# Kernel tuning notes

Hardware: AMD Instinct MI355X
Metric: run time of the kernel (lower is better)

The kernel has to match this reference:

```python
import jax, jax.numpy as jnp
import numpy as np

RADIUS = 2
TEMP = 1.0
B, CIN, D, H, W = 1, 32, 64, 64, 64
PROJ, OUT = 64, 64
K = (2 * RADIUS + 1) ** 3  # 125 local offsets

_OFFSETS = np.array([(dz, dy, dx)
                     for dz in range(-RADIUS, RADIUS + 1)
                     for dy in range(-RADIUS, RADIUS + 1)
                     for dx in range(-RADIUS, RADIUS + 1)], dtype=np.int32)


def _conv3d(x, w, b, pad):
    y = jax.lax.conv_general_dilated(
        x, w, window_strides=(1, 1, 1), padding=[(pad, pad)] * 3,
        dimension_numbers=('NCDHW', 'OIDHW', 'NCDHW'))
    if b is not None:
        y = y + b[None, :, None, None, None]
    return y


def _l2norm(x):
    # torch F.normalize(dim=1): x / max(||x||_2, 1e-12)
    n = jnp.sqrt(jnp.sum(x * x, axis=1, keepdims=True))
    return x / jnp.maximum(n, 1e-12)


def _inorm(x, eps=1e-5):
    # InstanceNorm3d (affine=False): normalize over spatial dims per (B,C)
    mu = jnp.mean(x, axis=(2, 3, 4), keepdims=True)
    var = jnp.mean((x - mu) ** 2, axis=(2, 3, 4), keepdims=True)
    return (x - mu) * jax.lax.rsqrt(var + eps)


def _ntn(x):
    return jnp.nan_to_num(x, nan=0.0, posinf=0.0, neginf=0.0)


def setup_inputs() -> dict:
    key = jax.random.key(0)
    ks = jax.random.split(key, 8)
    s = 0.05
    return {
        'source_features': jax.random.normal(ks[0], (B, CIN, D, H, W), jnp.float32),
        'warped_target_features': jax.random.normal(ks[1], (B, CIN, D, H, W), jnp.float32),
        'w_src': jax.random.normal(ks[2], (PROJ, CIN, 1, 1, 1), jnp.float32) * s,
        'b_src': jnp.zeros((PROJ,), jnp.float32),
        'w_tgt': jax.random.normal(ks[3], (PROJ, CIN, 1, 1, 1), jnp.float32) * s,
        'b_tgt': jnp.zeros((PROJ,), jnp.float32),
        'w_enc1': jax.random.normal(ks[4], (OUT, K + 5, 3, 3, 3), jnp.float32) * s,
        'b_enc1': jnp.zeros((OUT,), jnp.float32),
        'w_enc2': jax.random.normal(ks[5], (OUT, OUT, 3, 3, 3), jnp.float32) * s,
        'b_enc2': jnp.zeros((OUT,), jnp.float32),
    }


def reference(source_features, warped_target_features, w_src, b_src, w_tgt, b_tgt,
              w_enc1, b_enc1, w_enc2, b_enc2):
    sp = _l2norm(_conv3d(source_features, w_src, b_src, 0))      # [B,P,D,H,W]
    tp = _l2norm(_conv3d(warped_target_features, w_tgt, b_tgt, 0))
    pt = jnp.pad(tp, ((0, 0), (0, 0), (RADIUS, RADIUS), (RADIUS, RADIUS), (RADIUS, RADIUS)),
                 mode='edge')  # replicate pad

    starts = jnp.asarray(_OFFSETS + RADIUS, jnp.int32)  # [K,3] slice starts

    def corr_one(st):
        sh = jax.lax.dynamic_slice(pt, (0, 0, st[0], st[1], st[2]), (B, PROJ, D, H, W))
        return jnp.sum(sp * sh, axis=1)  # [B,D,H,W]

    corr = jnp.transpose(jax.vmap(corr_one)(starts), (1, 0, 2, 3, 4))  # [B,K,D,H,W]
    scaled = corr / max(TEMP, 1e-6)

    top2 = jax.lax.top_k(jnp.moveaxis(scaled, 1, -1), 2)[0]  # [B,D,H,W,2]
    m = jnp.moveaxis(top2[..., 0:1], -1, 1)   # running max   [B,1,D,H,W]
    s2 = jnp.moveaxis(top2[..., 1:2], -1, 1)  # second max

    p = jnp.exp(scaled - m)                    # [B,K,D,H,W]
    Z = jnp.sum(p, axis=1, keepdims=True)
    inv = 1.0 / jnp.maximum(Z, 1e-8)

    offv = jnp.asarray(_OFFSETS, jnp.float32)  # [K,3]
    expected_offset = _ntn(jnp.einsum('bkdhw,kc->bcdhw', p, offv) * inv)
    confidence = _ntn(jnp.minimum(inv, 1.0))   # max-prob = exp(m-m)/Z
    second_prob = jnp.exp(s2 - m) * inv
    margin = _ntn(jnp.maximum(confidence - second_prob, 0.0))
    entropy = _ntn(m + jnp.log(jnp.maximum(Z, 1e-8))
                   - jnp.sum(p * scaled, axis=1, keepdims=True) * inv)

    enc_in = jnp.concatenate([corr, expected_offset, confidence, entropy], axis=1)  # [B,K+5,D,H,W]
    h = _conv3d(enc_in, w_enc1, b_enc1, 1)
    h = jax.nn.gelu(_inorm(h), approximate=False)
    h = _conv3d(h, w_enc2, b_enc2, 1)
    h = jax.nn.gelu(_inorm(h), approximate=False)
    encoded_features = _ntn(h)

    return expected_offset, confidence, margin, entropy, encoded_features
```

## Files before the change

kernel.cpp:

```cpp
#include <hip/hip_runtime.h>

#define DEV __device__ __forceinline__

typedef short bf16x8 __attribute__((ext_vector_type(8)));
typedef float f32x4 __attribute__((ext_vector_type(4)));
typedef float f32x16 __attribute__((ext_vector_type(16)));

static const int NVOX = 262144;

DEV float bflo(unsigned int u) { return __uint_as_float(u << 16); }
DEV float bfhi(unsigned int u) { return __uint_as_float(u & 0xffff0000u); }
DEV float bf2f(unsigned short s) { return __uint_as_float(((unsigned int)s) << 16); }
DEV unsigned short f2bf(float f) {
    unsigned int x = __float_as_uint(f);
    x += 0x7fffu + ((x >> 16) & 1u);
    return (unsigned short)(x >> 16);
}
DEV float ldin(const void* p, int i, int f) {
    return f ? ((const float*)p)[i] : bf2f(((const unsigned short*)p)[i]);
}

DEV void gld16(const unsigned short* g, unsigned short* l) {
    __builtin_amdgcn_global_load_lds(
        (const __attribute__((address_space(1))) unsigned int*)g,
        (__attribute__((address_space(3))) unsigned int*)l, 16, 0, 0);
}

__global__ void sniff_kernel(const unsigned short* __restrict__ src, int* __restrict__ flag) {
    __shared__ int cnt[256];
    int t = threadIdx.x;
    int c = 0;
    for (int i = t; i < 4096; i += 256) {
        unsigned int u = (unsigned int)src[i] & 0x7fffu;
        c += (u >= 0x4900u) ? 1 : 0;
    }
    cnt[t] = c;
    __syncthreads();
    for (int s = 128; s > 0; s >>= 1) {
        if (t < s) cnt[t] += cnt[t + s];
        __syncthreads();
    }
    if (t == 0) *flag = (cnt[0] > 8) ? 1 : 0;
}

__global__ void prep_kernel(const void* __restrict__ w1, const void* __restrict__ w2,
                            const void* __restrict__ bsv, const void* __restrict__ btv,
                            const void* __restrict__ b1v, const void* __restrict__ b2v,
                            const int* __restrict__ flag,
                            unsigned short* __restrict__ Wf1,
                            unsigned short* __restrict__ Wf2,
                            float* __restrict__ fbias) {
    const int f = *flag;
    int idx = blockIdx.x * 256 + threadIdx.x;
    const int N1  = 27 * 8 * 2 * 512;
    const int N1E = 4 * 2 * 512;
    const int N2  = 27 * 4 * 2 * 512;
    if (idx < N1) {
        int frag = idx >> 9;
        int r    = idx & 511;
        int lane = r >> 3, j = r & 7;
        int nt = frag & 1;
        int tk = frag >> 1;
        int tap = tk >> 3, kc = tk & 7;
        int o  = nt * 32 + (lane & 31);
        int cp = kc * 16 + (lane >> 5) * 8 + j;
        Wf1[idx] = f2bf(ldin(w1, (o * 130 + cp) * 27 + tap, f));
    } else if (idx < N1 + N1E) {
        int i2 = idx - N1;
        int frag = i2 >> 9;
        int r    = i2 & 511;
        int lane = r >> 3, j = r & 7;
        int nt = frag & 1, kc = frag >> 1;
        int o   = nt * 32 + (lane & 31);
        int kap = kc * 16 + (lane >> 5) * 8 + j;
        unsigned short val = 0;
        if (kap < 54) {
            int tap = kap >> 1, ch = 128 + (kap & 1);
            val = f2bf(ldin(w1, (o * 130 + ch) * 27 + tap, f));
        }
        Wf1[idx] = val;
    } else if (idx < N1 + N1E + N2) {
        int i2 = idx - N1 - N1E;
        int frag = i2 >> 9;
        int r    = i2 & 511;
        int lane = r >> 3, j = r & 7;
        int nt = frag & 1;
        int tk = frag >> 1;
        int tap = tk >> 2, kc = tk & 3;
        int o = nt * 32 + (lane & 31);
        int c = kc * 16 + (lane >> 5) * 8 + j;
        Wf2[i2] = f2bf(ldin(w2, (o * 64 + c) * 27 + tap, f));
    } else if (idx < N1 + N1E + N2 + 256) {
        int j = idx - N1 - N1E - N2;
        const void* bp = (j < 64) ? bsv : (j < 128) ? btv : (j < 192) ? b1v : b2v;
        fbias[j] = ldin(bp, j & 63, f);
    }
}

__global__ __launch_bounds__(256) void proj_kernel(
        const void* __restrict__ Xsrc, const void* __restrict__ Xtgt,
        const void* __restrict__ Wsrc, const void* __restrict__ Wtgt,
        const float* __restrict__ fbias, const int* __restrict__ flag,
        unsigned short* __restrict__ SP, unsigned short* __restrict__ TP) {
    const int f = *flag;
    const void* Xin = blockIdx.y ? Xtgt : Xsrc;
    const void* W   = blockIdx.y ? Wtgt : Wsrc;
    const float* Bb = fbias + (blockIdx.y ? 64 : 0);
    unsigned short* Outp = blockIdx.y ? TP : SP;

    __shared__ float ws[2048];
    const int t = threadIdx.x;
    for (int i = t; i < 2048; i += 256) {
        int ci = i >> 6, o = i & 63;
        ws[i] = ldin(W, o * 32 + ci, f);
    }
    __syncthreads();

    const size_t v = (size_t)blockIdx.x * 256 + t;
    float acc[64];
#pragma unroll
    for (int o = 0; o < 64; ++o) acc[o] = Bb[o];
    if (f) {
        const float* Xf = (const float*)Xin;
        for (int ci = 0; ci < 32; ++ci) {
            float x = Xf[(size_t)ci * NVOX + v];
            const float4* wr = (const float4*)(ws + ci * 64);
#pragma unroll
            for (int o4 = 0; o4 < 16; ++o4) {
                float4 w4 = wr[o4];
                acc[o4 * 4 + 0] = fmaf(w4.x, x, acc[o4 * 4 + 0]);
                acc[o4 * 4 + 1] = fmaf(w4.y, x, acc[o4 * 4 + 1]);
                acc[o4 * 4 + 2] = fmaf(w4.z, x, acc[o4 * 4 + 2]);
                acc[o4 * 4 + 3] = fmaf(w4.w, x, acc[o4 * 4 + 3]);
            }
        }
    } else {
        const unsigned short* Xb = (const unsigned short*)Xin;
        for (int ci = 0; ci < 32; ++ci) {
            float x = bf2f(Xb[(size_t)ci * NVOX + v]);
            const float4* wr = (const float4*)(ws + ci * 64);
#pragma unroll
            for (int o4 = 0; o4 < 16; ++o4) {
                float4 w4 = wr[o4];
                acc[o4 * 4 + 0] = fmaf(w4.x, x, acc[o4 * 4 + 0]);
                acc[o4 * 4 + 1] = fmaf(w4.y, x, acc[o4 * 4 + 1]);
                acc[o4 * 4 + 2] = fmaf(w4.z, x, acc[o4 * 4 + 2]);
                acc[o4 * 4 + 3] = fmaf(w4.w, x, acc[o4 * 4 + 3]);
            }
        }
    }
    float s = 0.f;
#pragma unroll
    for (int o = 0; o < 64; ++o) s = fmaf(acc[o], acc[o], s);
    float scale = 1.f / fmaxf(sqrtf(s), 1e-12f);

    unsigned int pk[32];
#pragma unroll
    for (int o = 0; o < 32; ++o)
        pk[o] = (unsigned int)f2bf(acc[2 * o] * scale) |
                ((unsigned int)f2bf(acc[2 * o + 1] * scale) << 16);
    uint4* outp = (uint4*)(Outp + v * 64);
#pragma unroll
    for (int j = 0; j < 8; ++j)
        outp[j] = make_uint4(pk[4 * j], pk[4 * j + 1], pk[4 * j + 2], pk[4 * j + 3]);
}

__global__ __launch_bounds__(256) void corr_kernel(
        const unsigned short* __restrict__ SP, const unsigned short* __restrict__ TP,
        unsigned short* __restrict__ X1, float* __restrict__ Out) {
    __shared__ __align__(16) unsigned short tpb[2][80 * 64];
    __shared__ __align__(16) unsigned short sband[2][64 * 128];

    const int t = threadIdx.x;
    const int wv = t >> 6, lane = t & 63;
    const int q = lane >> 4, l16 = lane & 15;
    const int x0 = wv * 16;

    const int bid = blockIdx.x;
    const int wg = (bid & 7) * 256 + (bid >> 3);
    const int z = wg >> 5, y = (wg & 31) * 2;
    const size_t vb0 = ((size_t)z * 64 + y) * 64;
    const size_t vb1 = vb0 + 64;

    const unsigned short* ar0 = SP + (vb0 + x0 + l16) * 64 + q * 8;
    const unsigned short* ar1 = SP + (vb1 + x0 + l16) * 64 + q * 8;
    const bf16x8 a00 = *(const bf16x8*)(ar0);
    const bf16x8 a01 = *(const bf16x8*)(ar0 + 32);
    const bf16x8 a10 = *(const bf16x8*)(ar1);
    const bf16x8 a11 = *(const bf16x8*)(ar1 + 32);

    auto stage_tp = [&](int it, int b) {
        const int zc = min(max(z + it / 6 - 2, 0), 63);
        const int yc = min(max(y - 2 + it % 6, 0), 63);
        const unsigned short* tb = TP + ((size_t)zc * 64 + yc) * 4096;
#pragma unroll
        for (int j = 0; j < 2; ++j) {
            int c = t + j * 256;
            int pp = c >> 3, cc = c & 7;
            int xc = min(max(pp - 2, 0), 63);
            gld16(tb + xc * 64 + ((cc ^ (pp & 7)) * 8),
                  &tpb[b][(wv * 64 + j * 256) * 8]);
        }
        if (wv < 2) {
            int c = 512 + wv * 64 + lane;
            int pp = c >> 3, cc = c & 7;
            int xc = min(max(pp - 2, 0), 63);
            gld16(tb + xc * 64 + ((cc ^ (pp & 7)) * 8),
                  &tpb[b][(512 + wv * 64) * 8]);
        }
    };

    stage_tp(0, 0);
    __syncthreads();

    int p = 0;
    for (int it = 0; it < 30; ++it) {
        if (it < 29) stage_tp(it + 1, p ^ 1);
        const int dz = it / 6, j = it % 6;
        const bool r0 = (j < 5), r1 = (j > 0);

        f32x4 acc0[2] = {{0.f, 0.f, 0.f, 0.f}, {0.f, 0.f, 0.f, 0.f}};
        f32x4 acc1[2] = {{0.f, 0.f, 0.f, 0.f}, {0.f, 0.f, 0.f, 0.f}};
        {
            const char* tb = (const char*)tpb[p];
#pragma unroll
            for (int nt = 0; nt < 2; ++nt) {
                const int pr = x0 + nt * 16 + l16;
                bf16x8 b0 = *(const bf16x8*)(tb + pr * 128 + ((q ^ (pr & 7)) * 16));
                bf16x8 b1 = *(const bf16x8*)(tb + pr * 128 + (((4 + q) ^ (pr & 7)) * 16));
                if (r0) {
                    acc0[nt] = __builtin_amdgcn_mfma_f32_16x16x32_bf16(a00, b0, acc0[nt], 0, 0, 0);
                    acc0[nt] = __builtin_amdgcn_mfma_f32_16x16x32_bf16(a01, b1, acc0[nt], 0, 0, 0);
                }
                if (r1) {
                    acc1[nt] = __builtin_amdgcn_mfma_f32_16x16x32_bf16(a10, b0, acc1[nt], 0, 0, 0);
                    acc1[nt] = __builtin_amdgcn_mfma_f32_16x16x32_bf16(a11, b1, acc1[nt], 0, 0, 0);
                }
            }
        }
        if (r0) {
            const int kb = dz * 25 + j * 5;
            char* sg = (char*)sband[0];
#pragma unroll
            for (int nt = 0; nt < 2; ++nt)
#pragma unroll
                for (int r = 0; r < 4; ++r) {
                    int ml = q * 4 + r;
                    int dxp = nt * 16 + l16 - ml;
                    if ((unsigned)dxp < 5u) {
                        int xl = x0 + ml;
                        *(unsigned short*)(sg + xl * 256 + (((kb + dxp) * 2) ^ ((xl & 7) << 4))) =
                            f2bf(acc0[nt][r]);
                    }
                }
        }
        if (r1) {
            const int kb = dz * 25 + (j - 1) * 5;
            char* sg = (char*)sband[1];
#pragma unroll
            for (int nt = 0; nt < 2; ++nt)
#pragma unroll
                for (int r = 0; r < 4; ++r) {
                    int ml = q * 4 + r;
                    int dxp = nt * 16 + l16 - ml;
                    if ((unsigned)dxp < 5u) {
                        int xl = x0 + ml;
                        *(unsigned short*)(sg + xl * 256 + (((kb + dxp) * 2) ^ ((xl & 7) << 4))) =
                            f2bf(acc1[nt][r]);
                    }
                }
        }
        __syncthreads();
        p ^= 1;
    }

    for (int half = 0; half < 2; ++half) {
        const size_t vbase = half ? vb1 : vb0;
        const int vox = t >> 2, part = t & 3;
        const int sx = (vox & 7) << 4;
        const char* sg = (const char*)sband[half];
        uint4 u[4];
#pragma unroll
        for (int j = 0; j < 4; ++j)
            u[j] = *(const uint4*)(sg + vox * 256 + ((part * 64 + j * 16) ^ sx));

        float m = -1e30f, s2 = -1e30f;
#pragma unroll
        for (int j = 0; j < 4; ++j) {
            const unsigned int uu[4] = {u[j].x, u[j].y, u[j].z, u[j].w};
#pragma unroll
            for (int w = 0; w < 4; ++w) {
                int k = part * 32 + j * 8 + w * 2;
                float d0 = (k < 125) ? bflo(uu[w]) : -1e30f;
                float d1 = (k + 1 < 125) ? bfhi(uu[w]) : -1e30f;
                float lo0 = fminf(d0, m); m = fmaxf(d0, m); s2 = fmaxf(s2, lo0);
                float lo1 = fminf(d1, m); m = fmaxf(d1, m); s2 = fmaxf(s2, lo1);
            }
        }
#pragma unroll
        for (int off = 1; off <= 2; off <<= 1) {
            float om = __shfl_xor(m, off, 64);
            float os = __shfl_xor(s2, off, 64);
            float lo = fminf(m, om);
            m = fmaxf(m, om);
            s2 = fmaxf(fmaxf(s2, os), lo);
        }
        int kk = part * 32;
        int dz0 = kk / 25, rem = kk - dz0 * 25, dy0 = rem / 5, dx0 = rem - dy0 * 5;
        float fx = (float)(dx0 - 2), fy = (float)(dy0 - 2), fz = (float)(dz0 - 2);
        float Zs = 0.f, S1 = 0.f, Ox = 0.f, Oy = 0.f, Oz = 0.f;
#pragma unroll
        for (int j = 0; j < 4; ++j) {
            const unsigned int uu[4] = {u[j].x, u[j].y, u[j].z, u[j].w};
#pragma unroll
            for (int w = 0; w < 8; ++w) {
                int k = part * 32 + j * 8 + w;
                bool ok = (k < 125);
                float d = (w & 1) ? bfhi(uu[w >> 1]) : bflo(uu[w >> 1]);
                d = ok ? d : 0.f;
                float e = ok ? __expf(d - m) : 0.f;
                Zs += e; S1 = fmaf(e, d, S1);
                Ox = fmaf(e, fx, Ox); Oy = fmaf(e, fy, Oy); Oz = fmaf(e, fz, Oz);
                fx += 1.f;
                if (fx > 2.5f) { fx = -2.f; fy += 1.f; if (fy > 2.5f) { fy = -2.f; fz += 1.f; } }
            }
        }
#pragma unroll
        for (int off = 1; off <= 2; off <<= 1) {
            Zs += __shfl_xor(Zs, off, 64);
            S1 += __shfl_xor(S1, off, 64);
            Ox += __shfl_xor(Ox, off, 64);
            Oy += __shfl_xor(Oy, off, 64);
            Oz += __shfl_xor(Oz, off, 64);
        }
        if (part == 0) {
            float inv  = 1.f / fmaxf(Zs, 1e-8f);
            float eoz = Oz * inv, eoy = Oy * inv, eox = Ox * inv;
            float conf = fminf(inv, 1.f);
            float marg = fmaxf(conf - __expf(s2 - m) * inv, 0.f);
            float ent  = m + __logf(fmaxf(Zs, 1e-8f)) - S1 * inv;
            char* sgw = (char*)sband[half];
            *(unsigned short*)(sgw + vox * 256 + (250 ^ sx)) = f2bf(eoz);
            *(unsigned short*)(sgw + vox * 256 + (252 ^ sx)) = f2bf(eoy);
            *(unsigned short*)(sgw + vox * 256 + (254 ^ sx)) = f2bf(eox);
            const size_t v = vbase + vox;
            *(unsigned int*)(X1 + v * 160 + 128) =
                (unsigned int)f2bf(conf) | ((unsigned int)f2bf(ent) << 16);
            Out[v]                    = eoz;
            Out[(size_t)NVOX + v]     = eoy;
            Out[(size_t)2 * NVOX + v] = eox;
            Out[(size_t)3 * NVOX + v] = conf;
            Out[(size_t)4 * NVOX + v] = marg;
            Out[(size_t)5 * NVOX + v] = ent;
        }
    }
    __syncthreads();

#pragma unroll
    for (int j = 0; j < 8; ++j) {
        int i = t + j * 256;
        int row = i >> 10, rr = i & 1023;
        int vox = rr >> 4, cc = rr & 15;
        *(uint4*)(X1 + ((row ? vb1 : vb0) + vox) * 160 + (size_t)cc * 8) =
            *(const uint4*)((const char*)sband[row] + vox * 256 + ((cc * 16) ^ ((vox & 7) << 4)));
    }
}

template <int XSTRIDE, int CPAD, int KC, int NLD, int MINW, bool TAIL>
__global__ __launch_bounds__(256, MINW) void conv3_kernel(
        const unsigned short* __restrict__ Xin, const unsigned short* __restrict__ Wf,
        const unsigned short* __restrict__ Wfe,
        const float* __restrict__ Bias, unsigned short* __restrict__ Out) {
    constexpr int SLOT = 66 * CPAD;
    constexpr int CH16 = CPAD / 8;
    __shared__ __align__(16) unsigned short lds[3 * SLOT];
    const int lin = blockIdx.x;
    const int wg = (lin & 7) * 256 + (lin >> 3);
    const int z = wg >> 5;
    const int y = (wg & 31) * 2;
    const int t = threadIdx.x;
    const int wv = t >> 6, lane = t & 63;
    const int ry = wv & 1;
    const int nt = wv >> 1;
    const int l31 = lane & 31, kh = lane >> 5;

    f32x16 acc[2] = {};

    auto stage_plane = [&](int pidx) {
        const int zz = z + (pidx >> 2) - 1;
        const int py = y + (pidx & 3) - 1;
        if ((unsigned)zz >= 64u || (unsigned)py >= 64u) return;
        const unsigned short* base = Xin + (((size_t)zz * 64 + py) * 64) * XSTRIDE;
        unsigned short* dst = lds + (pidx % 3) * SLOT + CPAD;
#pragma unroll
        for (int i = 0; i < NLD; ++i) {
            int chunk = wv * 64 + lane + i * 256;
            int xi = chunk / CH16;
            int cc = chunk % CH16;
            gld16(base + xi * XSTRIDE + ((cc ^ ((xi + 1) & 7)) * 8),
                  dst + (size_t)(wv * 64 + i * 256) * 8);
        }
    };

    if (TAIL) {
        unsigned short* ebuf = lds;
#pragma unroll
        for (int i2 = 0; i2 < 16; ++i2) {
            int i = t + i2 * 256;
            int vox = i >> 5, slot = i & 31;
            unsigned int val = 0u;
            int kap;
            if (slot < 27) {
                int ddz = slot / 9 - 1, ddy = (slot / 3) % 3 - 1, dxx = slot % 3 - 1;
                int zz = z + ddz, yy = y + (vox >> 6) + ddy, xx = (vox & 63) + dxx;
                kap = slot * 2;
                if ((unsigned)zz < 64u && (unsigned)yy < 64u && (unsigned)xx < 64u)
                    val = *(const unsigned int*)(Xin + (((size_t)zz * 64 + yy) * 64 + xx) * XSTRIDE + 128);
            } else {
                kap = 54 + (slot - 27) * 2;
            }
            *(unsigned int*)(ebuf + (size_t)vox * 72 + kap) = val;
        }
        __syncthreads();
#pragma unroll
        for (int kc = 0; kc < 4; ++kc) {
            bf16x8 bte = *(const bf16x8*)(Wfe + (size_t)(kc * 2 + nt) * 512 + lane * 8);
#pragma unroll
            for (int half = 0; half < 2; ++half) {
                bf16x8 a = *(const bf16x8*)(ebuf +
                    (size_t)((ry * 2 + half) * 32 + l31) * 72 + kc * 16 + kh * 8);
                acc[half] = __builtin_amdgcn_mfma_f32_32x32x16_bf16(a, bte, acc[half], 0, 0, 0);
            }
        }
        __syncthreads();
    }

    if (t < 6 * CH16) {
        int sl = t / (2 * CH16), r2 = (t / CH16) & 1, c = t % CH16;
        *(uint4*)(&lds[(size_t)sl * SLOT + (size_t)(r2 * 65) * CPAD + c * 8]) =
            make_uint4(0u, 0u, 0u, 0u);
    }
    stage_plane(0);
    stage_plane(1);
    __syncthreads();

    for (int i = 0; i < 9; ++i) {
        const int s0 = (i / 3) * 4 + i % 3;
        if (i == 3 || i == 6) {
            stage_plane(s0 + 1);
            __syncthreads();
        }
        if (s0 + 2 < 12) stage_plane(s0 + 2);

        const int zz = z + i / 3 - 1;
        const int dy = i % 3 - 1;
        const bool ok = (unsigned)zz < 64u && (unsigned)(y + ry + dy) < 64u;
        const unsigned short* sb = lds + (size_t)((s0 + ry) % 3) * SLOT;
        if (ok) {
#pragma unroll
            for (int dx = 0; dx < 3; ++dx) {
                const int tap = (i / 3) * 9 + (i % 3) * 3 + dx;
                const unsigned short* wt = Wf + ((size_t)(tap * KC) * 2 + nt) * 512 + lane * 8;
                bf16x8 bf[KC];
#pragma unroll
                for (int kc = 0; kc < KC; ++kc)
                    bf[kc] = *(const bf16x8*)(wt + (size_t)kc * 2 * 512);
#pragma unroll
                for (int kc = 0; kc < KC; ++kc) {
#pragma unroll
                    for (int half = 0; half < 2; ++half) {
                        const int row = half * 32 + l31 + dx;
                        const int chunk = kc * 2 + kh;
                        bf16x8 a = *(const bf16x8*)(&sb[(size_t)row * CPAD +
                                                        ((chunk ^ (row & 7)) * 8)]);
                        acc[half] = __builtin_amdgcn_mfma_f32_32x32x16_bf16(a, bf[kc], acc[half], 0, 0, 0);
                    }
                }
            }
        }
        __syncthreads();
    }

    const size_t vb = ((size_t)z * 64 + (y + ry)) * 64;
    const int oc = nt * 32 + l31;
    const float bv = Bias[oc];
#pragma unroll
    for (int half = 0; half < 2; ++half) {
#pragma unroll
        for (int reg = 0; reg < 16; ++reg) {
            int x = half * 32 + (reg & 3) + 8 * (reg >> 2) + 4 * kh;
            Out[(vb + x) * 64 + oc] = f2bf(acc[half][reg] + bv);
        }
    }
}

__global__ __launch_bounds__(256) void stats_kernel(
        const unsigned short* __restrict__ H, float* __restrict__ stats) {
    const int t = threadIdx.x;
    const int c = t & 63, g = t >> 6;
    float s = 0.f, q = 0.f;
    for (int v = blockIdx.x * 4 + g; v < NVOX; v += gridDim.x * 4) {
        float x = bf2f(H[(size_t)v * 64 + c]);
        s += x; q = fmaf(x, x, q);
    }
    __shared__ float ls[256], lq[256];
    ls[t] = s; lq[t] = q;
    __syncthreads();
    if (t < 64) {
        s = ls[t] + ls[t + 64] + ls[t + 128] + ls[t + 192];
        q = lq[t] + lq[t + 64] + lq[t + 128] + lq[t + 192];
        atomicAdd(&stats[c], s);
        atomicAdd(&stats[64 + c], q);
    }
}

__global__ void finalize_kernel(const float* __restrict__ stats, float* __restrict__ musr) {
    int c = threadIdx.x;
    if (c < 64) {
        float mu  = stats[c] * (1.0f / 262144.0f);
        float var = stats[64 + c] * (1.0f / 262144.0f) - mu * mu;
        musr[c] = mu;
        musr[64 + c] = rsqrtf(var + 1e-5f);
    }
}

__global__ __launch_bounds__(256) void norm_gelu_kernel(
        const unsigned short* __restrict__ H, const float* __restrict__ musr,
        unsigned short* __restrict__ G) {
    const size_t base = ((size_t)blockIdx.x * 256 + threadIdx.x) * 8;
    uint4 u = *(const uint4*)(H + base);
    const int c0 = (int)(base & 63);
    const unsigned int uu[4] = {u.x, u.y, u.z, u.w};
    unsigned int w[4];
#pragma unroll
    for (int p = 0; p < 4; ++p) {
        int c = c0 + p * 2;
        float x0 = (bflo(uu[p]) - musr[c]) * musr[64 + c];
        float x1 = (bfhi(uu[p]) - musr[c + 1]) * musr[64 + c + 1];
        float g0 = 0.5f * x0 * (1.f + erff(x0 * 0.70710678118f));
        float g1 = 0.5f * x1 * (1.f + erff(x1 * 0.70710678118f));
        w[p] = (unsigned int)f2bf(g0) | ((unsigned int)f2bf(g1) << 16);
    }
    *(uint4*)(G + base) = make_uint4(w[0], w[1], w[2], w[3]);
}

__global__ __launch_bounds__(256) void out_final_kernel(
        const unsigned short* __restrict__ H2, const float* __restrict__ musr,
        float* __restrict__ OutEnc) {
    __shared__ float tile[64 * 260];
    const int t = threadIdx.x;
    const size_t v0 = (size_t)blockIdx.x * 256;
#pragma unroll
    for (int i = 0; i < 8; ++i) {
        int chunk = t + i * 256;
        uint4 u = *(const uint4*)(H2 + v0 * 64 + (size_t)chunk * 8);
        int vox = chunk >> 3;
        int c0 = (chunk & 7) * 8;
        const unsigned int uu[4] = {u.x, u.y, u.z, u.w};
#pragma unroll
        for (int p = 0; p < 4; ++p) {
            int c = c0 + p * 2;
            float x0 = (bflo(uu[p]) - musr[c]) * musr[64 + c];
            float x1 = (bfhi(uu[p]) - musr[c + 1]) * musr[64 + c + 1];
            tile[c * 260 + vox]       = 0.5f * x0 * (1.f + erff(x0 * 0.70710678118f));
            tile[(c + 1) * 260 + vox] = 0.5f * x1 * (1.f + erff(x1 * 0.70710678118f));
        }
    }
    __syncthreads();
    const int c = t >> 2, sub = t & 3;
#pragma unroll
    for (int iter = 0; iter < 16; ++iter) {
        int fq = iter * 4 + sub;
        float4 val = *(const float4*)(&tile[c * 260 + fq * 4]);
        *(float4*)(OutEnc + (size_t)c * NVOX + v0 + fq * 4) = val;
    }
}

extern "C" void kernel_launch(void* const* d_in, const int* in_sizes, int n_in,
                              void* d_out, int out_size, void* d_ws, size_t ws_size,
                              hipStream_t stream) {
    const void* src  = d_in[0];
    const void* tgt  = d_in[1];
    const void* wsrc = d_in[2];
    const void* bsrc = d_in[3];
    const void* wtgt = d_in[4];
    const void* btgt = d_in[5];
    const void* w1   = d_in[6];
    const void* b1   = d_in[7];
    const void* w2   = d_in[8];
    const void* b2   = d_in[9];
    float* out = (float*)d_out;

    char* ws = (char*)d_ws;
    unsigned short* TPb = (unsigned short*)(ws);
    unsigned short* SPb = (unsigned short*)(ws + 33554432);
    unsigned short* X1  = (unsigned short*)(ws + 67108864);
    unsigned short* Wf1 = (unsigned short*)(ws + 150994944);
    unsigned short* Wf2 = (unsigned short*)(ws + 151547904);
    int*   flag   = (int*)  (ws + 151769088);
    float* fbias  = (float*)(ws + 151769152);
    float* stats1 = (float*)(ws + 151770176);
    float* musr1  = (float*)(ws + 151770688);
    float* stats2 = (float*)(ws + 151771200);
    float* musr2  = (float*)(ws + 151771712);
    unsigned short* H1 = SPb;
    unsigned short* G1 = TPb;
    unsigned short* H2 = X1;
    unsigned short* Wf1e = Wf1 + 27 * 8 * 2 * 512;

    (void)hipMemsetAsync(stats1, 0, 2048, stream);
    sniff_kernel<<<1, 256, 0, stream>>>((const unsigned short*)src, flag);
    prep_kernel<<<1313, 256, 0, stream>>>(w1, w2, bsrc, btgt, b1, b2, flag, Wf1, Wf2, fbias);
    proj_kernel<<<dim3(1024, 2), 256, 0, stream>>>(src, tgt, wsrc, wtgt, fbias, flag, SPb, TPb);
    corr_kernel<<<2048, 256, 0, stream>>>(SPb, TPb, X1, out);
    conv3_kernel<160, 128, 8, 4, 3, true><<<2048, 256, 0, stream>>>(X1, Wf1, Wf1e, fbias + 128, H1);
    stats_kernel<<<256, 256, 0, stream>>>(H1, stats1);
    finalize_kernel<<<1, 64, 0, stream>>>(stats1, musr1);
    norm_gelu_kernel<<<8192, 256, 0, stream>>>(H1, musr1, G1);
    conv3_kernel<64, 64, 4, 2, 4, false><<<2048, 256, 0, stream>>>(G1, Wf2, nullptr, fbias + 192, H2);
    stats_kernel<<<256, 256, 0, stream>>>(H2, stats2);
    finalize_kernel<<<1, 64, 0, stream>>>(stats2, musr2);
    out_final_kernel<<<1024, 256, 0, stream>>>(H2, musr2, out + 6 * (size_t)NVOX);
}
```

Measured before the change: 713.1 us.

## Run projection on MFMA with split-bf16 and fuse norm stats into conv epilogue

```diff
diff --git a/kernel.cpp b/kernel.cpp
--- a/kernel.cpp
+++ b/kernel.cpp
@@ -44,17 +44,20 @@
 }
 
 __global__ void prep_kernel(const void* __restrict__ w1, const void* __restrict__ w2,
+                            const void* __restrict__ wsv, const void* __restrict__ wtv,
                             const void* __restrict__ bsv, const void* __restrict__ btv,
                             const void* __restrict__ b1v, const void* __restrict__ b2v,
                             const int* __restrict__ flag,
                             unsigned short* __restrict__ Wf1,
                             unsigned short* __restrict__ Wf2,
+                            unsigned short* __restrict__ Wp,
                             float* __restrict__ fbias) {
     const int f = *flag;
     int idx = blockIdx.x * 256 + threadIdx.x;
     const int N1  = 27 * 8 * 2 * 512;
     const int N1E = 4 * 2 * 512;
     const int N2  = 27 * 4 * 2 * 512;
+    const int N3  = 16 * 512;
     if (idx < N1) {
         int frag = idx >> 9;
         int r    = idx & 511;
@@ -94,75 +97,101 @@
         int j = idx - N1 - N1E - N2;
         const void* bp = (j < 64) ? bsv : (j < 128) ? btv : (j < 192) ? b1v : b2v;
         fbias[j] = ldin(bp, j & 63, f);
+    } else if (idx < N1 + N1E + N2 + 256 + N3) {
+        int i3 = idx - (N1 + N1E + N2 + 256);
+        int frag = i3 >> 9;
+        int r    = i3 & 511;
+        int lane = r >> 3, j = r & 7;
+        int hl = frag & 1, kc = (frag >> 1) & 1, nt = (frag >> 2) & 1, pj = frag >> 3;
+        const void* wp = pj ? wtv : wsv;
+        int oc = nt * 32 + (lane & 31);
+        int ci = kc * 16 + (lane >> 5) * 8 + j;
+        float val = ldin(wp, oc * 32 + ci, f);
+        unsigned short hi = f2bf(val);
+        Wp[i3] = hl ? f2bf(val - bf2f(hi)) : hi;
     }
 }
 
 __global__ __launch_bounds__(256) void proj_kernel(
         const void* __restrict__ Xsrc, const void* __restrict__ Xtgt,
-        const void* __restrict__ Wsrc, const void* __restrict__ Wtgt,
+        const unsigned short* __restrict__ Wp,
         const float* __restrict__ fbias, const int* __restrict__ flag,
         unsigned short* __restrict__ SP, unsigned short* __restrict__ TP) {
     const int f = *flag;
-    const void* Xin = blockIdx.y ? Xtgt : Xsrc;
-    const void* W   = blockIdx.y ? Wtgt : Wsrc;
-    const float* Bb = fbias + (blockIdx.y ? 64 : 0);
-    unsigned short* Outp = blockIdx.y ? TP : SP;
-
-    __shared__ float ws[2048];
+    const int pj = blockIdx.y;
+    const void* Xin = pj ? Xtgt : Xsrc;
+    const float* Bb = fbias + (pj ? 64 : 0);
+    unsigned short* Outp = pj ? TP : SP;
+    const unsigned short* Wpp = Wp + pj * 4096;
+
     const int t = threadIdx.x;
-    for (int i = t; i < 2048; i += 256) {
-        int ci = i >> 6, o = i & 63;
-        ws[i] = ldin(W, o * 32 + ci, f);
-    }
-    __syncthreads();
-
-    const size_t v = (size_t)blockIdx.x * 256 + t;
-    float acc[64];
-#pragma unroll
-    for (int o = 0; o < 64; ++o) acc[o] = Bb[o];
-    if (f) {
-        const float* Xf = (const float*)Xin;
-        for (int ci = 0; ci < 32; ++ci) {
-            float x = Xf[(size_t)ci * NVOX + v];
-            const float4* wr = (const float4*)(ws + ci * 64);
-#pragma unroll
-            for (int o4 = 0; o4 < 16; ++o4) {
-                float4 w4 = wr[o4];
-                acc[o4 * 4 + 0] = fmaf(w4.x, x, acc[o4 * 4 + 0]);
-                acc[o4 * 4 + 1] = fmaf(w4.y, x, acc[o4 * 4 + 1]);
-                acc[o4 * 4 + 2] = fmaf(w4.z, x, acc[o4 * 4 + 2]);
-                acc[o4 * 4 + 3] = fmaf(w4.w, x, acc[o4 * 4 + 3]);
-            }
-        }
-    } else {
-        const unsigned short* Xb = (const unsigned short*)Xin;
-        for (int ci = 0; ci < 32; ++ci) {
-            float x = bf2f(Xb[(size_t)ci * NVOX + v]);
-            const float4* wr = (const float4*)(ws + ci * 64);
-#pragma unroll
-            for (int o4 = 0; o4 < 16; ++o4) {
-                float4 w4 = wr[o4];
-                acc[o4 * 4 + 0] = fmaf(w4.x, x, acc[o4 * 4 + 0]);
-                acc[o4 * 4 + 1] = fmaf(w4.y, x, acc[o4 * 4 + 1]);
-                acc[o4 * 4 + 2] = fmaf(w4.z, x, acc[o4 * 4 + 2]);
-                acc[o4 * 4 + 3] = fmaf(w4.w, x, acc[o4 * 4 + 3]);
-            }
-        }
-    }
-    float s = 0.f;
-#pragma unroll
-    for (int o = 0; o < 64; ++o) s = fmaf(acc[o], acc[o], s);
-    float scale = 1.f / fmaxf(sqrtf(s), 1e-12f);
-
-    unsigned int pk[32];
-#pragma unroll
-    for (int o = 0; o < 32; ++o)
-        pk[o] = (unsigned int)f2bf(acc[2 * o] * scale) |
-                ((unsigned int)f2bf(acc[2 * o + 1] * scale) << 16);
-    uint4* outp = (uint4*)(Outp + v * 64);
-#pragma unroll
-    for (int j = 0; j < 8; ++j)
-        outp[j] = make_uint4(pk[4 * j], pk[4 * j + 1], pk[4 * j + 2], pk[4 * j + 3]);
+    const int wv = t >> 6, lane = t & 63;
+    const int l31 = lane & 31, kh = lane >> 5;
+    const size_t mbase = (size_t)blockIdx.x * 256 + wv * 64;
+
+    bf16x8 bw[2][2][2];
+#pragma unroll
+    for (int nt = 0; nt < 2; ++nt)
+#pragma unroll
+        for (int kc = 0; kc < 2; ++kc)
+#pragma unroll
+            for (int hl = 0; hl < 2; ++hl)
+                bw[nt][kc][hl] = *(const bf16x8*)(Wpp + (size_t)(((nt * 2 + kc) * 2 + hl)) * 512 + lane * 8);
+
+    bf16x8 ah[2][2], al[2][2];
+#pragma unroll
+    for (int mt = 0; mt < 2; ++mt)
+#pragma unroll
+        for (int kc = 0; kc < 2; ++kc) {
+            const int vx = (int)(mbase + mt * 32 + l31);
+#pragma unroll
+            for (int j = 0; j < 8; ++j) {
+                int ci = kc * 16 + kh * 8 + j;
+                float xv = ldin(Xin, ci * NVOX + vx, f);
+                unsigned short hi = f2bf(xv);
+                ah[mt][kc][j] = (short)hi;
+                al[mt][kc][j] = (short)f2bf(xv - bf2f(hi));
+            }
+        }
+
+    f32x16 acc[2][2] = {};
+#pragma unroll
+    for (int mt = 0; mt < 2; ++mt)
+#pragma unroll
+        for (int kc = 0; kc < 2; ++kc)
+#pragma unroll
+            for (int nt = 0; nt < 2; ++nt) {
+                acc[mt][nt] = __builtin_amdgcn_mfma_f32_32x32x16_bf16(ah[mt][kc], bw[nt][kc][0], acc[mt][nt], 0, 0, 0);
+                acc[mt][nt] = __builtin_amdgcn_mfma_f32_32x32x16_bf16(al[mt][kc], bw[nt][kc][0], acc[mt][nt], 0, 0, 0);
+                acc[mt][nt] = __builtin_amdgcn_mfma_f32_32x32x16_bf16(ah[mt][kc], bw[nt][kc][1], acc[mt][nt], 0, 0, 0);
+            }
+
+    const float b0 = Bb[l31], b1 = Bb[32 + l31];
+#pragma unroll
+    for (int mt = 0; mt < 2; ++mt) {
+        f32x16 s;
+#pragma unroll
+        for (int reg = 0; reg < 16; ++reg) {
+            float a0 = acc[mt][0][reg] + b0;
+            float a1 = acc[mt][1][reg] + b1;
+            acc[mt][0][reg] = a0;
+            acc[mt][1][reg] = a1;
+            s[reg] = fmaf(a0, a0, a1 * a1);
+        }
+#pragma unroll
+        for (int off = 1; off <= 16; off <<= 1)
+#pragma unroll
+            for (int reg = 0; reg < 16; ++reg)
+                s[reg] += __shfl_xor(s[reg], off, 64);
+#pragma unroll
+        for (int reg = 0; reg < 16; ++reg) {
+            float sc = 1.f / fmaxf(sqrtf(s[reg]), 1e-12f);
+            int row = (reg & 3) + 8 * (reg >> 2) + 4 * kh;
+            size_t v = mbase + mt * 32 + row;
+            Outp[v * 64 + l31]      = f2bf(acc[mt][0][reg] * sc);
+            Outp[v * 64 + 32 + l31] = f2bf(acc[mt][1][reg] * sc);
+        }
+    }
 }
 
 __global__ __launch_bounds__(256) void corr_kernel(
@@ -370,7 +399,8 @@
 __global__ __launch_bounds__(256, MINW) void conv3_kernel(
         const unsigned short* __restrict__ Xin, const unsigned short* __restrict__ Wf,
         const unsigned short* __restrict__ Wfe,
-        const float* __restrict__ Bias, unsigned short* __restrict__ Out) {
+        const float* __restrict__ Bias, unsigned short* __restrict__ Out,
+        float* __restrict__ Stats) {
     constexpr int SLOT = 66 * CPAD;
     constexpr int CH16 = CPAD / 8;
     __shared__ __align__(16) unsigned short lds[3 * SLOT];
@@ -484,33 +514,23 @@
     const size_t vb = ((size_t)z * 64 + (y + ry)) * 64;
     const int oc = nt * 32 + l31;
     const float bv = Bias[oc];
+    float ssum = 0.f, sq = 0.f;
 #pragma unroll
     for (int half = 0; half < 2; ++half) {
 #pragma unroll
         for (int reg = 0; reg < 16; ++reg) {
             int x = half * 32 + (reg & 3) + 8 * (reg >> 2) + 4 * kh;
-            Out[(vb + x) * 64 + oc] = f2bf(acc[half][reg] + bv);
-        }
-    }
-}
-
-__global__ __launch_bounds__(256) void stats_kernel(
-        const unsigned short* __restrict__ H, float* __restrict__ stats) {
-    const int t = threadIdx.x;
-    const int c = t & 63, g = t >> 6;
-    float s = 0.f, q = 0.f;
-    for (int v = blockIdx.x * 4 + g; v < NVOX; v += gridDim.x * 4) {
-        float x = bf2f(H[(size_t)v * 64 + c]);
-        s += x; q = fmaf(x, x, q);
-    }
-    __shared__ float ls[256], lq[256];
-    ls[t] = s; lq[t] = q;
-    __syncthreads();
-    if (t < 64) {
-        s = ls[t] + ls[t + 64] + ls[t + 128] + ls[t + 192];
-        q = lq[t] + lq[t + 64] + lq[t + 128] + lq[t + 192];
-        atomicAdd(&stats[c], s);
-        atomicAdd(&stats[64 + c], q);
+            unsigned short us = f2bf(acc[half][reg] + bv);
+            Out[(vb + x) * 64 + oc] = us;
+            float xv = bf2f(us);
+            ssum += xv; sq = fmaf(xv, xv, sq);
+        }
+    }
+    ssum += __shfl_xor(ssum, 32, 64);
+    sq   += __shfl_xor(sq, 32, 64);
+    if (kh == 0) {
+        atomicAdd(&Stats[oc], ssum);
+        atomicAdd(&Stats[64 + oc], sq);
     }
 }
 
@@ -607,18 +627,18 @@
     unsigned short* G1 = TPb;
     unsigned short* H2 = X1;
     unsigned short* Wf1e = Wf1 + 27 * 8 * 2 * 512;
+    unsigned short* Wp   = Wf1 + 27 * 8 * 2 * 512 + 4 * 2 * 512;
 
     (void)hipMemsetAsync(stats1, 0, 2048, stream);
     sniff_kernel<<<1, 256, 0, stream>>>((const unsigned short*)src, flag);
-    prep_kernel<<<1313, 256, 0, stream>>>(w1, w2, bsrc, btgt, b1, b2, flag, Wf1, Wf2, fbias);
-    proj_kernel<<<dim3(1024, 2), 256, 0, stream>>>(src, tgt, wsrc, wtgt, fbias, flag, SPb, TPb);
+    prep_kernel<<<1345, 256, 0, stream>>>(w1, w2, wsrc, wtgt, bsrc, btgt, b1, b2,
+                                          flag, Wf1, Wf2, Wp, fbias);
+    proj_kernel<<<dim3(1024, 2), 256, 0, stream>>>(src, tgt, Wp, fbias, flag, SPb, TPb);
     corr_kernel<<<2048, 256, 0, stream>>>(SPb, TPb, X1, out);
-    conv3_kernel<160, 128, 8, 4, 3, true><<<2048, 256, 0, stream>>>(X1, Wf1, Wf1e, fbias + 128, H1);
-    stats_kernel<<<256, 256, 0, stream>>>(H1, stats1);
+    conv3_kernel<160, 128, 8, 4, 3, true><<<2048, 256, 0, stream>>>(X1, Wf1, Wf1e, fbias + 128, H1, stats1);
     finalize_kernel<<<1, 64, 0, stream>>>(stats1, musr1);
     norm_gelu_kernel<<<8192, 256, 0, stream>>>(H1, musr1, G1);
-    conv3_kernel<64, 64, 4, 2, 4, false><<<2048, 256, 0, stream>>>(G1, Wf2, nullptr, fbias + 192, H2);
-    stats_kernel<<<256, 256, 0, stream>>>(H2, stats2);
+    conv3_kernel<64, 64, 4, 2, 4, false><<<2048, 256, 0, stream>>>(G1, Wf2, nullptr, fbias + 192, H2, stats2);
     finalize_kernel<<<1, 64, 0, stream>>>(stats2, musr2);
     out_final_kernel<<<1024, 256, 0, stream>>>(H2, musr2, out + 6 * (size_t)NVOX);
 }
```

Result: slower. 790.1 us (+10.8%).
